# Kernel tuning notes

Hardware: AMD Instinct MI355X
Metric: run time of the kernel (lower is better)

## Reference

```python
import jax, jax.numpy as jnp
import numpy as np

LN_EPS = 1e-5
NORM_EPS = 1e-12
SLOPE = 0.1

def _layernorm(x, g, b):
    m = jnp.mean(x, axis=-1, keepdims=True)
    v = jnp.mean(jnp.square(x - m), axis=-1, keepdims=True)
    return (x - m) * jax.lax.rsqrt(v + LN_EPS) * g + b

def _leaky(x):
    return jnp.where(x >= 0, x, SLOPE * x)

def setup_inputs() -> dict:
    key = jax.random.key(0)
    ks = jax.random.split(key, 8)
    N = 1048576
    features = jax.random.normal(ks[0], (N, 128), dtype=jnp.float32)
    # PyTorch Linear default init: U(-1/sqrt(fan_in), 1/sqrt(fan_in))
    W1 = jax.random.uniform(ks[1], (32, 128), jnp.float32, -1/np.sqrt(128), 1/np.sqrt(128))
    g1 = jnp.ones((32,), jnp.float32); b1 = jnp.zeros((32,), jnp.float32)
    W2 = jax.random.uniform(ks[2], (16, 32), jnp.float32, -1/np.sqrt(32), 1/np.sqrt(32))
    g2 = jnp.ones((16,), jnp.float32); b2 = jnp.zeros((16,), jnp.float32)
    W3 = jax.random.uniform(ks[3], (3, 16), jnp.float32, -1/np.sqrt(16), 1/np.sqrt(16))
    b3 = jax.random.uniform(ks[4], (3,), jnp.float32, -1/np.sqrt(16), 1/np.sqrt(16))
    return {"features": features, "W1": W1, "g1": g1, "b1": b1,
            "W2": W2, "g2": g2, "b2": b2, "W3": W3, "b3": b3}

def reference(features, W1, g1, b1, W2, g2, b2, W3, b3):
    x = features @ W1.T                       # [N,32]
    x = _leaky(_layernorm(x, g1, b1))
    x = x @ W2.T                               # [N,16]
    x = _leaky(_layernorm(x, g2, b2))
    x = x @ W3.T + b3                          # [N,3]
    # F.normalize(dim=-1): x / max(||x||_2, eps)
    n = jnp.linalg.norm(x, axis=-1, keepdims=True)
    return x / jnp.maximum(n, NORM_EPS)
```

## Files before the change

kernel.cpp:

```cpp
#include <hip/hip_runtime.h>
#include <math.h>

typedef short bf16x8 __attribute__((ext_vector_type(8)));
typedef float f32x4  __attribute__((ext_vector_type(4)));

#define TPB 256
#define ROWS 256
#define CSTRIDE 36
#define BFR_BYTES 16384
#define CT_BYTES (ROWS * CSTRIDE * 4)
#define BOFF(nt, ks, p) ((((nt)*4 + (ks))*2 + (p))*256)
#define GRID 768

#define WBAR() do { asm volatile("s_waitcnt lgkmcnt(0)" ::: "memory"); \
                    __builtin_amdgcn_s_barrier(); } while (0)

__device__ __forceinline__ unsigned cvt_pk_bf16(float lo, float hi) {
    unsigned r;
    asm("v_cvt_pk_bf16_f32 %0, %1, %2" : "=v"(r) : "v"(lo), "v"(hi));
    return r;
}

__device__ __forceinline__ void split2pk(float x0, float x1, unsigned &p, unsigned &q) {
    p = cvt_pk_bf16(x0, x1);
    const float f0 = __uint_as_float(p << 16);
    const float f1 = __uint_as_float(p & 0xffff0000u);
    q = cvt_pk_bf16(x0 - f0, x1 - f1);
}

__global__ __launch_bounds__(TPB, 3) void decoder_kernel(
    const float* __restrict__ feat,
    const float* __restrict__ W1, const float* __restrict__ g1, const float* __restrict__ b1,
    const float* __restrict__ W2, const float* __restrict__ g2, const float* __restrict__ b2,
    const float* __restrict__ W3, const float* __restrict__ b3,
    float* __restrict__ out, int N,
    unsigned* __restrict__ ctr, unsigned nchunks)
{
    __shared__ __align__(16) unsigned char lds[BFR_BYTES + CT_BYTES + 16];
    unsigned* bfr = (unsigned*)lds;
    float*    Ct  = (float*)(lds + BFR_BYTES);
    volatile unsigned* nxt_sh = (volatile unsigned*)(lds + BFR_BYTES + CT_BYTES);

    const int t = threadIdx.x;
    const int l = t & 63;
    const int w = t >> 6;
    const int arow = l & 15;
    const int acol = (l >> 4) * 8;

    for (int c = t; c < 512; c += 256) {
        const int lc = c & 63, ks = (c >> 6) & 3, nt = (c >> 8) & 1;
        const float* wp = W1 + (nt * 16 + (lc & 15)) * 128 + ks * 32 + (lc >> 4) * 8;
        float v[8];
        *(float4*)(v)     = *(const float4*)(wp);
        *(float4*)(v + 4) = *(const float4*)(wp + 4);
        unsigned p[4], q[4];
#pragma unroll
        for (int i = 0; i < 4; ++i) split2pk(v[2*i], v[2*i+1], p[i], q[i]);
        uint4 q1 = {p[0], p[1], p[2], p[3]};
        uint4 q2 = {q[0], q[1], q[2], q[3]};
        *(uint4*)(bfr + BOFF(nt, ks, 0) + lc * 4) = q1;
        *(uint4*)(bfr + BOFF(nt, ks, 1) + lc * 4) = q2;
    }
    if (t == 0) *nxt_sh = atomicAdd(ctr, 1u);
    __syncthreads();
    unsigned cur = *nxt_sh;

    float4 buf[2][8];
    if (cur < nchunks) {
        size_t rr = (size_t)cur * ROWS + (size_t)w * 64 + arow;
        if (rr >= (size_t)N) rr = N - 1;
        const float* ap = feat + rr * 128 + acol;
#pragma unroll
        for (int ks = 0; ks < 4; ++ks) {
            buf[0][2 * ks]     = *(const float4*)(ap + ks * 32);
            buf[0][2 * ks + 1] = *(const float4*)(ap + ks * 32 + 4);
        }
    }

    while (cur < nchunks) {
        const size_t blk0 = (size_t)cur * ROWS;

#pragma unroll
        for (int j = 0; j < 4; ++j) {
            if (j == 1 && t == 0) *nxt_sh = atomicAdd(ctr, 1u);
            if (j < 3) {
                size_t rr = blk0 + (size_t)w * 64 + (j + 1) * 16 + arow;
                if (rr >= (size_t)N) rr = N - 1;
                const float* ap = feat + rr * 128 + acol;
#pragma unroll
                for (int ks = 0; ks < 4; ++ks) {
                    buf[(j + 1) & 1][2 * ks]     = *(const float4*)(ap + ks * 32);
                    buf[(j + 1) & 1][2 * ks + 1] = *(const float4*)(ap + ks * 32 + 4);
                }
            }
            f32x4 acc0 = {0.f, 0.f, 0.f, 0.f};
            f32x4 acc1 = {0.f, 0.f, 0.f, 0.f};
#pragma unroll
            for (int ks = 0; ks < 4; ++ks) {
                float v[8];
                *(float4*)(v)     = buf[j & 1][2 * ks];
                *(float4*)(v + 4) = buf[j & 1][2 * ks + 1];
                unsigned p[4], q[4];
#pragma unroll
                for (int i = 0; i < 4; ++i) split2pk(v[2*i], v[2*i+1], p[i], q[i]);
                uint4 q1 = {p[0], p[1], p[2], p[3]};
                uint4 q2 = {q[0], q[1], q[2], q[3]};
                bf16x8 a1 = __builtin_bit_cast(bf16x8, q1);
                bf16x8 a2 = __builtin_bit_cast(bf16x8, q2);
                bf16x8 B10 = __builtin_bit_cast(bf16x8, *(const uint4*)(bfr + BOFF(0, ks, 0) + l * 4));
                bf16x8 B20 = __builtin_bit_cast(bf16x8, *(const uint4*)(bfr + BOFF(0, ks, 1) + l * 4));
                bf16x8 B11 = __builtin_bit_cast(bf16x8, *(const uint4*)(bfr + BOFF(1, ks, 0) + l * 4));
                bf16x8 B21 = __builtin_bit_cast(bf16x8, *(const uint4*)(bfr + BOFF(1, ks, 1) + l * 4));
                acc0 = __builtin_amdgcn_mfma_f32_16x16x32_bf16(a1, B10, acc0, 0, 0, 0);
                acc1 = __builtin_amdgcn_mfma_f32_16x16x32_bf16(a1, B11, acc1, 0, 0, 0);
                acc0 = __builtin_amdgcn_mfma_f32_16x16x32_bf16(a2, B10, acc0, 0, 0, 0);
                acc1 = __builtin_amdgcn_mfma_f32_16x16x32_bf16(a2, B11, acc1, 0, 0, 0);
                acc0 = __builtin_amdgcn_mfma_f32_16x16x32_bf16(a1, B20, acc0, 0, 0, 0);
                acc1 = __builtin_amdgcn_mfma_f32_16x16x32_bf16(a1, B21, acc1, 0, 0, 0);
            }
            const int crow = w * 64 + j * 16 + (l >> 4) * 4;
            const int ccol = l & 15;
#pragma unroll
            for (int r = 0; r < 4; ++r) {
                Ct[(crow + r) * CSTRIDE + ccol]      = acc0[r];
                Ct[(crow + r) * CSTRIDE + 16 + ccol] = acc1[r];
            }
        }
        WBAR();

        float x[32];
#pragma unroll
        for (int c = 0; c < 8; ++c)
            *(float4*)(x + c * 4) = *(const float4*)(Ct + t * CSTRIDE + c * 4);
        const unsigned nxt = *nxt_sh;
        WBAR();

        if (nxt < nchunks) {
            size_t rr = (size_t)nxt * ROWS + (size_t)w * 64 + arow;
            if (rr >= (size_t)N) rr = N - 1;
            const float* ap = feat + rr * 128 + acol;
#pragma unroll
            for (int ks = 0; ks < 4; ++ks) {
                buf[0][2 * ks]     = *(const float4*)(ap + ks * 32);
                buf[0][2 * ks + 1] = *(const float4*)(ap + ks * 32 + 4);
            }
        }

        float m = 0.f;
#pragma unroll
        for (int j = 0; j < 32; ++j) m += x[j];
        m *= (1.f / 32.f);
        float var = 0.f;
#pragma unroll
        for (int j = 0; j < 32; ++j) { const float d = x[j] - m; var = fmaf(d, d, var); }
        var *= (1.f / 32.f);
        const float rs1 = rsqrtf(var + 1e-5f);

        float z[32];
#pragma unroll
        for (int j = 0; j < 32; ++j) {
            float y = (x[j] - m) * rs1 * g1[j] + b1[j];
            z[j] = (y >= 0.f) ? y : 0.1f * y;
        }

        float a2v[16];
#pragma unroll
        for (int k = 0; k < 16; ++k) {
            const float* __restrict__ wrow = W2 + k * 32;
            float s = 0.f;
#pragma unroll
            for (int j = 0; j < 32; ++j) s = fmaf(z[j], wrow[j], s);
            a2v[k] = s;
        }

        float m2 = 0.f;
#pragma unroll
        for (int k = 0; k < 16; ++k) m2 += a2v[k];
        m2 *= (1.f / 16.f);
        float v2 = 0.f;
#pragma unroll
        for (int k = 0; k < 16; ++k) { const float d = a2v[k] - m2; v2 = fmaf(d, d, v2); }
        v2 *= (1.f / 16.f);
        const float rs2 = rsqrtf(v2 + 1e-5f);

        float z2[16];
#pragma unroll
        for (int k = 0; k < 16; ++k) {
            float y = (a2v[k] - m2) * rs2 * g2[k] + b2[k];
            z2[k] = (y >= 0.f) ? y : 0.1f * y;
        }

        float o[3];
#pragma unroll
        for (int q = 0; q < 3; ++q) {
            const float* __restrict__ wrow = W3 + q * 16;
            float s = b3[q];
#pragma unroll
            for (int k = 0; k < 16; ++k) s = fmaf(z2[k], wrow[k], s);
            o[q] = s;
        }
        const float nrm = sqrtf(o[0]*o[0] + o[1]*o[1] + o[2]*o[2]);
        const float inv = 1.f / fmaxf(nrm, 1e-12f);

        const size_t myrow = blk0 + t;
        if (myrow < (size_t)N) {
            out[myrow * 3 + 0] = o[0] * inv;
            out[myrow * 3 + 1] = o[1] * inv;
            out[myrow * 3 + 2] = o[2] * inv;
        }

        cur = nxt;
    }
}

extern "C" void kernel_launch(void* const* d_in, const int* in_sizes, int n_in,
                              void* d_out, int out_size, void* d_ws, size_t ws_size,
                              hipStream_t stream) {
    const float* feat = (const float*)d_in[0];
    const float* W1   = (const float*)d_in[1];
    const float* g1   = (const float*)d_in[2];
    const float* b1   = (const float*)d_in[3];
    const float* W2   = (const float*)d_in[4];
    const float* g2   = (const float*)d_in[5];
    const float* b2   = (const float*)d_in[6];
    const float* W3   = (const float*)d_in[7];
    const float* b3   = (const float*)d_in[8];
    float* out = (float*)d_out;

    const int N = in_sizes[0] / 128;
    const unsigned nchunks = (unsigned)((N + ROWS - 1) / ROWS);
    unsigned* ctr = (unsigned*)d_ws;

    hipMemsetAsync(ctr, 0, sizeof(unsigned), stream);
    decoder_kernel<<<GRID, TPB, 0, stream>>>(feat, W1, g1, b1, W2, g2, b2, W3, b3,
                                             out, N, ctr, nchunks);
}
```

Before: 125.3 us.

## Replace persistent atomic work-stealing loop with one-block-per-tile grid

New measurement: 120.7 us. 3.7% less time.

```diff
diff --git a/kernel.cpp b/kernel.cpp
--- a/kernel.cpp
+++ b/kernel.cpp
@@ -5,22 +5,16 @@
 typedef float f32x4  __attribute__((ext_vector_type(4)));
 
 #define TPB 256
-#define ROWS 256
 #define CSTRIDE 36
 #define BFR_BYTES 16384
-#define CT_BYTES (ROWS * CSTRIDE * 4)
+#define CT_BYTES (256 * CSTRIDE * 4)
 #define BOFF(nt, ks, p) ((((nt)*4 + (ks))*2 + (p))*256)
-#define GRID 768
-
-#define WBAR() do { asm volatile("s_waitcnt lgkmcnt(0)" ::: "memory"); \
-                    __builtin_amdgcn_s_barrier(); } while (0)
 
 __device__ __forceinline__ unsigned cvt_pk_bf16(float lo, float hi) {
     unsigned r;
     asm("v_cvt_pk_bf16_f32 %0, %1, %2" : "=v"(r) : "v"(lo), "v"(hi));
     return r;
 }
-
 __device__ __forceinline__ void split2pk(float x0, float x1, unsigned &p, unsigned &q) {
     p = cvt_pk_bf16(x0, x1);
     const float f0 = __uint_as_float(p << 16);
@@ -33,19 +27,31 @@
     const float* __restrict__ W1, const float* __restrict__ g1, const float* __restrict__ b1,
     const float* __restrict__ W2, const float* __restrict__ g2, const float* __restrict__ b2,
     const float* __restrict__ W3, const float* __restrict__ b3,
-    float* __restrict__ out, int N,
-    unsigned* __restrict__ ctr, unsigned nchunks)
+    float* __restrict__ out, int N)
 {
-    __shared__ __align__(16) unsigned char lds[BFR_BYTES + CT_BYTES + 16];
+    __shared__ __align__(16) unsigned char lds[BFR_BYTES + CT_BYTES];
     unsigned* bfr = (unsigned*)lds;
-    float*    Ct  = (float*)(lds + BFR_BYTES);
-    volatile unsigned* nxt_sh = (volatile unsigned*)(lds + BFR_BYTES + CT_BYTES);
 
     const int t = threadIdx.x;
     const int l = t & 63;
     const int w = t >> 6;
     const int arow = l & 15;
     const int acol = (l >> 4) * 8;
+    float* myCt = (float*)(lds + BFR_BYTES) + w * 64 * CSTRIDE;
+
+    const size_t rows0 = (size_t)blockIdx.x * 256 + (size_t)w * 64;
+
+    float4 buf[2][8];
+    {
+        size_t rr = rows0 + arow;
+        if (rr >= (size_t)N) rr = N - 1;
+        const float* ap = feat + rr * 128 + acol;
+#pragma unroll
+        for (int ks = 0; ks < 4; ++ks) {
+            buf[0][2 * ks]     = *(const float4*)(ap + ks * 32);
+            buf[0][2 * ks + 1] = *(const float4*)(ap + ks * 32 + 4);
+        }
+    }
 
     for (int c = t; c < 512; c += 256) {
         const int lc = c & 63, ks = (c >> 6) & 3, nt = (c >> 8) & 1;
@@ -61,155 +67,120 @@
         *(uint4*)(bfr + BOFF(nt, ks, 0) + lc * 4) = q1;
         *(uint4*)(bfr + BOFF(nt, ks, 1) + lc * 4) = q2;
     }
-    if (t == 0) *nxt_sh = atomicAdd(ctr, 1u);
     __syncthreads();
-    unsigned cur = *nxt_sh;
-
-    float4 buf[2][8];
-    if (cur < nchunks) {
-        size_t rr = (size_t)cur * ROWS + (size_t)w * 64 + arow;
-        if (rr >= (size_t)N) rr = N - 1;
-        const float* ap = feat + rr * 128 + acol;
-#pragma unroll
-        for (int ks = 0; ks < 4; ++ks) {
-            buf[0][2 * ks]     = *(const float4*)(ap + ks * 32);
-            buf[0][2 * ks + 1] = *(const float4*)(ap + ks * 32 + 4);
-        }
-    }
-
-    while (cur < nchunks) {
-        const size_t blk0 = (size_t)cur * ROWS;
-
-#pragma unroll
-        for (int j = 0; j < 4; ++j) {
-            if (j == 1 && t == 0) *nxt_sh = atomicAdd(ctr, 1u);
-            if (j < 3) {
-                size_t rr = blk0 + (size_t)w * 64 + (j + 1) * 16 + arow;
-                if (rr >= (size_t)N) rr = N - 1;
-                const float* ap = feat + rr * 128 + acol;
-#pragma unroll
-                for (int ks = 0; ks < 4; ++ks) {
-                    buf[(j + 1) & 1][2 * ks]     = *(const float4*)(ap + ks * 32);
-                    buf[(j + 1) & 1][2 * ks + 1] = *(const float4*)(ap + ks * 32 + 4);
-                }
-            }
-            f32x4 acc0 = {0.f, 0.f, 0.f, 0.f};
-            f32x4 acc1 = {0.f, 0.f, 0.f, 0.f};
-#pragma unroll
-            for (int ks = 0; ks < 4; ++ks) {
-                float v[8];
-                *(float4*)(v)     = buf[j & 1][2 * ks];
-                *(float4*)(v + 4) = buf[j & 1][2 * ks + 1];
-                unsigned p[4], q[4];
-#pragma unroll
-                for (int i = 0; i < 4; ++i) split2pk(v[2*i], v[2*i+1], p[i], q[i]);
-                uint4 q1 = {p[0], p[1], p[2], p[3]};
-                uint4 q2 = {q[0], q[1], q[2], q[3]};
-                bf16x8 a1 = __builtin_bit_cast(bf16x8, q1);
-                bf16x8 a2 = __builtin_bit_cast(bf16x8, q2);
-                bf16x8 B10 = __builtin_bit_cast(bf16x8, *(const uint4*)(bfr + BOFF(0, ks, 0) + l * 4));
-                bf16x8 B20 = __builtin_bit_cast(bf16x8, *(const uint4*)(bfr + BOFF(0, ks, 1) + l * 4));
-                bf16x8 B11 = __builtin_bit_cast(bf16x8, *(const uint4*)(bfr + BOFF(1, ks, 0) + l * 4));
-                bf16x8 B21 = __builtin_bit_cast(bf16x8, *(const uint4*)(bfr + BOFF(1, ks, 1) + l * 4));
-                acc0 = __builtin_amdgcn_mfma_f32_16x16x32_bf16(a1, B10, acc0, 0, 0, 0);
-                acc1 = __builtin_amdgcn_mfma_f32_16x16x32_bf16(a1, B11, acc1, 0, 0, 0);
-                acc0 = __builtin_amdgcn_mfma_f32_16x16x32_bf16(a2, B10, acc0, 0, 0, 0);
-                acc1 = __builtin_amdgcn_mfma_f32_16x16x32_bf16(a2, B11, acc1, 0, 0, 0);
-                acc0 = __builtin_amdgcn_mfma_f32_16x16x32_bf16(a1, B20, acc0, 0, 0, 0);
-                acc1 = __builtin_amdgcn_mfma_f32_16x16x32_bf16(a1, B21, acc1, 0, 0, 0);
-            }
-            const int crow = w * 64 + j * 16 + (l >> 4) * 4;
-            const int ccol = l & 15;
-#pragma unroll
-            for (int r = 0; r < 4; ++r) {
-                Ct[(crow + r) * CSTRIDE + ccol]      = acc0[r];
-                Ct[(crow + r) * CSTRIDE + 16 + ccol] = acc1[r];
-            }
-        }
-        WBAR();
-
-        float x[32];
-#pragma unroll
-        for (int c = 0; c < 8; ++c)
-            *(float4*)(x + c * 4) = *(const float4*)(Ct + t * CSTRIDE + c * 4);
-        const unsigned nxt = *nxt_sh;
-        WBAR();
-
-        if (nxt < nchunks) {
-            size_t rr = (size_t)nxt * ROWS + (size_t)w * 64 + arow;
+
+#pragma unroll
+    for (int j = 0; j < 4; ++j) {
+        if (j < 3) {
+            size_t rr = rows0 + (j + 1) * 16 + arow;
             if (rr >= (size_t)N) rr = N - 1;
             const float* ap = feat + rr * 128 + acol;
 #pragma unroll
             for (int ks = 0; ks < 4; ++ks) {
-                buf[0][2 * ks]     = *(const float4*)(ap + ks * 32);
-                buf[0][2 * ks + 1] = *(const float4*)(ap + ks * 32 + 4);
+                buf[(j + 1) & 1][2 * ks]     = *(const float4*)(ap + ks * 32);
+                buf[(j + 1) & 1][2 * ks + 1] = *(const float4*)(ap + ks * 32 + 4);
             }
         }
-
-        float m = 0.f;
-#pragma unroll
-        for (int j = 0; j < 32; ++j) m += x[j];
-        m *= (1.f / 32.f);
-        float var = 0.f;
-#pragma unroll
-        for (int j = 0; j < 32; ++j) { const float d = x[j] - m; var = fmaf(d, d, var); }
-        var *= (1.f / 32.f);
-        const float rs1 = rsqrtf(var + 1e-5f);
-
-        float z[32];
-#pragma unroll
-        for (int j = 0; j < 32; ++j) {
-            float y = (x[j] - m) * rs1 * g1[j] + b1[j];
-            z[j] = (y >= 0.f) ? y : 0.1f * y;
-        }
-
-        float a2v[16];
-#pragma unroll
-        for (int k = 0; k < 16; ++k) {
-            const float* __restrict__ wrow = W2 + k * 32;
-            float s = 0.f;
-#pragma unroll
-            for (int j = 0; j < 32; ++j) s = fmaf(z[j], wrow[j], s);
-            a2v[k] = s;
-        }
-
-        float m2 = 0.f;
-#pragma unroll
-        for (int k = 0; k < 16; ++k) m2 += a2v[k];
-        m2 *= (1.f / 16.f);
-        float v2 = 0.f;
-#pragma unroll
-        for (int k = 0; k < 16; ++k) { const float d = a2v[k] - m2; v2 = fmaf(d, d, v2); }
-        v2 *= (1.f / 16.f);
-        const float rs2 = rsqrtf(v2 + 1e-5f);
-
-        float z2[16];
-#pragma unroll
-        for (int k = 0; k < 16; ++k) {
-            float y = (a2v[k] - m2) * rs2 * g2[k] + b2[k];
-            z2[k] = (y >= 0.f) ? y : 0.1f * y;
-        }
-
-        float o[3];
-#pragma unroll
-        for (int q = 0; q < 3; ++q) {
-            const float* __restrict__ wrow = W3 + q * 16;
-            float s = b3[q];
-#pragma unroll
-            for (int k = 0; k < 16; ++k) s = fmaf(z2[k], wrow[k], s);
-            o[q] = s;
-        }
-        const float nrm = sqrtf(o[0]*o[0] + o[1]*o[1] + o[2]*o[2]);
-        const float inv = 1.f / fmaxf(nrm, 1e-12f);
-
-        const size_t myrow = blk0 + t;
-        if (myrow < (size_t)N) {
-            out[myrow * 3 + 0] = o[0] * inv;
-            out[myrow * 3 + 1] = o[1] * inv;
-            out[myrow * 3 + 2] = o[2] * inv;
-        }
-
-        cur = nxt;
+        f32x4 acc0 = {0.f, 0.f, 0.f, 0.f};
+        f32x4 acc1 = {0.f, 0.f, 0.f, 0.f};
+#pragma unroll
+        for (int ks = 0; ks < 4; ++ks) {
+            float v[8];
+            *(float4*)(v)     = buf[j & 1][2 * ks];
+            *(float4*)(v + 4) = buf[j & 1][2 * ks + 1];
+            unsigned p[4], q[4];
+#pragma unroll
+            for (int i = 0; i < 4; ++i) split2pk(v[2*i], v[2*i+1], p[i], q[i]);
+            uint4 q1 = {p[0], p[1], p[2], p[3]};
+            uint4 q2 = {q[0], q[1], q[2], q[3]};
+            bf16x8 a1 = __builtin_bit_cast(bf16x8, q1);
+            bf16x8 a2 = __builtin_bit_cast(bf16x8, q2);
+            bf16x8 B10 = __builtin_bit_cast(bf16x8, *(const uint4*)(bfr + BOFF(0, ks, 0) + l * 4));
+            bf16x8 B20 = __builtin_bit_cast(bf16x8, *(const uint4*)(bfr + BOFF(0, ks, 1) + l * 4));
+            bf16x8 B11 = __builtin_bit_cast(bf16x8, *(const uint4*)(bfr + BOFF(1, ks, 0) + l * 4));
+            bf16x8 B21 = __builtin_bit_cast(bf16x8, *(const uint4*)(bfr + BOFF(1, ks, 1) + l * 4));
+            acc0 = __builtin_amdgcn_mfma_f32_16x16x32_bf16(a1, B10, acc0, 0, 0, 0);
+            acc1 = __builtin_amdgcn_mfma_f32_16x16x32_bf16(a1, B11, acc1, 0, 0, 0);
+            acc0 = __builtin_amdgcn_mfma_f32_16x16x32_bf16(a2, B10, acc0, 0, 0, 0);
+            acc1 = __builtin_amdgcn_mfma_f32_16x16x32_bf16(a2, B11, acc1, 0, 0, 0);
+            acc0 = __builtin_amdgcn_mfma_f32_16x16x32_bf16(a1, B20, acc0, 0, 0, 0);
+            acc1 = __builtin_amdgcn_mfma_f32_16x16x32_bf16(a1, B21, acc1, 0, 0, 0);
+        }
+        const int crow = j * 16 + (l >> 4) * 4;
+        const int ccol = l & 15;
+#pragma unroll
+        for (int r = 0; r < 4; ++r) {
+            myCt[(crow + r) * CSTRIDE + ccol]      = acc0[r];
+            myCt[(crow + r) * CSTRIDE + 16 + ccol] = acc1[r];
+        }
+    }
+
+    float x[32];
+#pragma unroll
+    for (int c = 0; c < 8; ++c)
+        *(float4*)(x + c * 4) = *(const float4*)(myCt + l * CSTRIDE + c * 4);
+
+    float m = 0.f;
+#pragma unroll
+    for (int j = 0; j < 32; ++j) m += x[j];
+    m *= (1.f / 32.f);
+    float var = 0.f;
+#pragma unroll
+    for (int j = 0; j < 32; ++j) { const float d = x[j] - m; var = fmaf(d, d, var); }
+    var *= (1.f / 32.f);
+    const float rs1 = rsqrtf(var + 1e-5f);
+
+    float z[32];
+#pragma unroll
+    for (int j = 0; j < 32; ++j) {
+        float y = (x[j] - m) * rs1 * g1[j] + b1[j];
+        z[j] = (y >= 0.f) ? y : 0.1f * y;
+    }
+
+    float a2v[16];
+#pragma unroll
+    for (int k = 0; k < 16; ++k) {
+        const float* __restrict__ wrow = W2 + k * 32;
+        float s = 0.f;
+#pragma unroll
+        for (int j = 0; j < 32; ++j) s = fmaf(z[j], wrow[j], s);
+        a2v[k] = s;
+    }
+
+    float m2 = 0.f;
+#pragma unroll
+    for (int k = 0; k < 16; ++k) m2 += a2v[k];
+    m2 *= (1.f / 16.f);
+    float v2 = 0.f;
+#pragma unroll
+    for (int k = 0; k < 16; ++k) { const float d = a2v[k] - m2; v2 = fmaf(d, d, v2); }
+    v2 *= (1.f / 16.f);
+    const float rs2 = rsqrtf(v2 + 1e-5f);
+
+    float z2[16];
+#pragma unroll
+    for (int k = 0; k < 16; ++k) {
+        float y = (a2v[k] - m2) * rs2 * g2[k] + b2[k];
+        z2[k] = (y >= 0.f) ? y : 0.1f * y;
+    }
+
+    float o[3];
+#pragma unroll
+    for (int q = 0; q < 3; ++q) {
+        const float* __restrict__ wrow = W3 + q * 16;
+        float s = b3[q];
+#pragma unroll
+        for (int k = 0; k < 16; ++k) s = fmaf(z2[k], wrow[k], s);
+        o[q] = s;
+    }
+    const float nrm = sqrtf(o[0]*o[0] + o[1]*o[1] + o[2]*o[2]);
+    const float inv = 1.f / fmaxf(nrm, 1e-12f);
+
+    const size_t myrow = rows0 + l;
+    if (myrow < (size_t)N) {
+        out[myrow * 3 + 0] = o[0] * inv;
+        out[myrow * 3 + 1] = o[1] * inv;
+        out[myrow * 3 + 2] = o[2] * inv;
     }
 }
 
@@ -228,10 +199,7 @@
     float* out = (float*)d_out;
 
     const int N = in_sizes[0] / 128;
-    const unsigned nchunks = (unsigned)((N + ROWS - 1) / ROWS);
-    unsigned* ctr = (unsigned*)d_ws;
-
-    hipMemsetAsync(ctr, 0, sizeof(unsigned), stream);
-    decoder_kernel<<<GRID, TPB, 0, stream>>>(feat, W1, g1, b1, W2, g2, b2, W3, b3,
-                                             out, N, ctr, nchunks);
-}
+    const int grid = (N + 255) / 256;
+
+    decoder_kernel<<<grid, TPB, 0, stream>>>(feat, W1, g1, b1, W2, g2, b2, W3, b3, out, N);
+}
```
